# Performance work log

Measured on AMD Instinct MI355X. Metric: run time of the kernel, lower is better.

Reference implementation:

```python
import jax, jax.numpy as jnp
import numpy as np

INPUT_DIM = 10              # number of binary covariates in x
N = 2_000_000               # batch size
C = 2 ** (INPUT_DIM + 1)    # 2048 (t, x) combinations, one Linear(1,1) each


def setup_inputs() -> dict:
    key = jax.random.key(0)
    kx, kt, ky, kw, kb = jax.random.split(key, 5)
    x = jax.random.randint(kx, (N, INPUT_DIM), 0, 2).astype(jnp.float32)  # binary covariates
    t = jax.random.randint(kt, (N, 1), 0, 2).astype(jnp.float32)          # binary treatment
    y = jax.random.normal(ky, (N, 1), dtype=jnp.float32)                  # outcome
    # Per-combination Linear(1,1): weight w[i] and bias b[i] for q_z_dummies[i]
    w = jax.random.normal(kw, (C,), dtype=jnp.float32) * 0.5
    b = jax.random.normal(kb, (C,), dtype=jnp.float32) * 0.5
    return {"x": x, "t": t, "y": y, "w": w, "b": b}


def reference(x, t, y, w, b):
    # The torch loop sums (w_i*y + b_i) * [exact match of (t, x) with combination i].
    # Exactly one combination matches per row, so this equals a gather at the
    # combination index. itertools.product([0,1], repeat=d+1) orders bits
    # (t, x_0, ..., x_{d-1}) with the FIRST bit most significant.
    powers = (2 ** jnp.arange(INPUT_DIM - 1, -1, -1)).astype(x.dtype)      # [d]
    idx = (t[:, 0] * (2 ** INPUT_DIM) + x @ powers).astype(jnp.int32)      # [N]
    z_logits = y * w[idx][:, None] + b[idx][:, None]                       # [N, 1]
    # Original returns (z_mu=0, z_var=0, z_logits) in binary mode; z_logits is
    # the only tensor output.
    return z_logits
```

## Files before the change

kernel.cpp:

```cpp
#include <hip/hip_runtime.h>
#include <hip/hip_bf16.h>


#define D          10
#define C_TAB      2048
#define TILE_ROWS  128
#define BLOCKS     1024
#define WPB        4

__device__ __forceinline__ void async_load16(const void* g, void* l) {
    __builtin_amdgcn_global_load_lds(
        (const __attribute__((address_space(1))) void*)g,
        (__attribute__((address_space(3))) void*)l, 16, 0, 0);
}

__device__ __forceinline__ int make_idx(const float* row, float tt) {
    const float2* p = (const float2*)row;
    float2 a0 = p[0], a1 = p[1], a2 = p[2], a3 = p[3], a4 = p[4];
    float v = a0.x;
    v = fmaf(v, 2.f, a0.y);
    v = fmaf(v, 2.f, a1.x);
    v = fmaf(v, 2.f, a1.y);
    v = fmaf(v, 2.f, a2.x);
    v = fmaf(v, 2.f, a2.y);
    v = fmaf(v, 2.f, a3.x);
    v = fmaf(v, 2.f, a3.y);
    v = fmaf(v, 2.f, a4.x);
    v = fmaf(v, 2.f, a4.y);
    v = fmaf(tt, 1024.f, v);
    return (int)v;
}

__global__ __launch_bounds__(256, 4) void enc_kernel(
    const float* __restrict__ x,
    const float* __restrict__ t,
    const float* __restrict__ y,
    const float* __restrict__ w,
    const float* __restrict__ b,
    float* __restrict__ out,
    int nTiles, int nTotalWaves)
{
    __shared__ float lw[C_TAB];
    __shared__ float lb[C_TAB];
    __shared__ float xs[WPB][TILE_ROWS * D];

    const int tid = threadIdx.x;

    {
        const float4* w4 = (const float4*)w;
        const float4* b4 = (const float4*)b;
        float4* lw4 = (float4*)lw;
        float4* lb4 = (float4*)lb;
        lw4[tid]       = w4[tid];
        lw4[tid + 256] = w4[tid + 256];
        lb4[tid]       = b4[tid];
        lb4[tid + 256] = b4[tid + 256];
    }
    __syncthreads();

    const int wave = tid >> 6;
    const int lane = tid & 63;
    float* xw = xs[wave];

    for (int tile = blockIdx.x * WPB + wave; tile < nTiles; tile += nTotalWaves) {
        const char* gbase = (const char*)x + (size_t)tile * (TILE_ROWS * D * 4);
        #pragma unroll
        for (int k = 0; k < 5; ++k) {
            async_load16(gbase + k * 1024 + lane * 16, (char*)xw + k * 1024);
        }

        const int r0 = tile * TILE_ROWS + lane;
        const int r1 = r0 + 64;
        float t0 = t[r0], t1 = t[r1];
        float y0 = y[r0], y1 = y[r1];

        __builtin_amdgcn_s_waitcnt(0);
        __asm__ volatile("" ::: "memory");

        const int i0 = make_idx(&xw[lane * D], t0);
        const int i1 = make_idx(&xw[(lane + 64) * D], t1);

        out[r0] = fmaf(y0, lw[i0], lb[i0]);
        out[r1] = fmaf(y1, lw[i1], lb[i1]);
    }
}

__global__ __launch_bounds__(256) void enc_tail(
    const float* __restrict__ x, const float* __restrict__ t,
    const float* __restrict__ y, const float* __restrict__ w,
    const float* __restrict__ b, float* __restrict__ out,
    int start, int n)
{
    int i = start + blockIdx.x * blockDim.x + threadIdx.x;
    if (i >= n) return;
    const float* r = x + (size_t)i * D;
    float v = r[0];
    #pragma unroll
    for (int j = 1; j < D; ++j) v = fmaf(v, 2.f, r[j]);
    int idx = (int)fmaf(t[i], 1024.f, v);
    out[i] = fmaf(y[i], w[idx], b[idx]);
}

extern "C" void kernel_launch(void* const* d_in, const int* in_sizes, int n_in,
                              void* d_out, int out_size, void* d_ws, size_t ws_size,
                              hipStream_t stream) {
    const float* x = (const float*)d_in[0];
    const float* t = (const float*)d_in[1];
    const float* y = (const float*)d_in[2];
    const float* w = (const float*)d_in[3];
    const float* b = (const float*)d_in[4];
    float* out = (float*)d_out;

    const int n = out_size;
    const int nTiles = n / TILE_ROWS;
    const int rem = n - nTiles * TILE_ROWS;

    enc_kernel<<<BLOCKS, 256, 0, stream>>>(x, t, y, w, b, out,
                                           nTiles, BLOCKS * WPB);
    if (rem > 0) {
        enc_tail<<<(rem + 255) / 256, 256, 0, stream>>>(
            x, t, y, w, b, out, nTiles * TILE_ROWS, n);
    }
}
```

Before: 134.9 us.

## Double-buffer x tile DMA loads and interleave w/b into float2 table

Each wave now prefetches the next tile of x into a second LDS buffer, along with its t and y values, while it computes the current tile. It waits on a partial vmcnt so that only the current tile's loads must finish. The weight and bias tables are interleaved into one float2 LDS array, so each lookup is a single LDS read instead of two. The cost is doubled per-wave LDS use and more live registers, and the launch bounds hint drops from 4 to 2. The partial-wait count also relies on a fixed number of outstanding memory operations per iteration.

```diff
diff --git a/kernel.cpp b/kernel.cpp
--- a/kernel.cpp
+++ b/kernel.cpp
@@ -2,13 +2,16 @@
 #include <hip/hip_bf16.h>
 
 
-#define D          10
-#define C_TAB      2048
-#define TILE_ROWS  128
-#define BLOCKS     1024
-#define WPB        4
+#define D        10
+#define TILE     128
+#define WPB      4
+#define BLOCKS   1024
+#define NTHREADS 256
 
-__device__ __forceinline__ void async_load16(const void* g, void* l) {
+#define WAITCNT_VM9 0x0F79
+#define WAITCNT_VM0 0x0F70
+
+__device__ __forceinline__ void dma16(const void* g, void* l) {
     __builtin_amdgcn_global_load_lds(
         (const __attribute__((address_space(1))) void*)g,
         (__attribute__((address_space(3))) void*)l, 16, 0, 0);
@@ -31,57 +34,85 @@
     return (int)v;
 }
 
-__global__ __launch_bounds__(256, 4) void enc_kernel(
+__global__ __launch_bounds__(NTHREADS, 2) void enc_kernel(
     const float* __restrict__ x,
     const float* __restrict__ t,
     const float* __restrict__ y,
     const float* __restrict__ w,
     const float* __restrict__ b,
     float* __restrict__ out,
-    int nTiles, int nTotalWaves)
+    int nTiles, int stride)
 {
-    __shared__ float lw[C_TAB];
-    __shared__ float lb[C_TAB];
-    __shared__ float xs[WPB][TILE_ROWS * D];
+    __shared__ float2 lwb[2048];
+    __shared__ float xs[WPB][2][TILE * D];
 
     const int tid = threadIdx.x;
 
     {
         const float4* w4 = (const float4*)w;
         const float4* b4 = (const float4*)b;
-        float4* lw4 = (float4*)lw;
-        float4* lb4 = (float4*)lb;
-        lw4[tid]       = w4[tid];
-        lw4[tid + 256] = w4[tid + 256];
-        lb4[tid]       = b4[tid];
-        lb4[tid + 256] = b4[tid + 256];
+        #pragma unroll
+        for (int k = 0; k < 2; ++k) {
+            float4 fw = w4[tid * 2 + k];
+            float4 fb = b4[tid * 2 + k];
+            int base = (tid * 2 + k) * 4;
+            lwb[base + 0] = make_float2(fw.x, fb.x);
+            lwb[base + 1] = make_float2(fw.y, fb.y);
+            lwb[base + 2] = make_float2(fw.z, fb.z);
+            lwb[base + 3] = make_float2(fw.w, fb.w);
+        }
     }
     __syncthreads();
 
     const int wave = tid >> 6;
     const int lane = tid & 63;
-    float* xw = xs[wave];
+    float* bufs[2] = { xs[wave][0], xs[wave][1] };
 
-    for (int tile = blockIdx.x * WPB + wave; tile < nTiles; tile += nTotalWaves) {
-        const char* gbase = (const char*)x + (size_t)tile * (TILE_ROWS * D * 4);
+    int tile = blockIdx.x * WPB + wave;
+    if (tile >= nTiles) return;
+
+    {
+        const char* g = (const char*)x + (size_t)tile * (TILE * D * 4);
         #pragma unroll
-        for (int k = 0; k < 5; ++k) {
-            async_load16(gbase + k * 1024 + lane * 16, (char*)xw + k * 1024);
+        for (int k = 0; k < 5; ++k)
+            dma16(g + k * 1024 + lane * 16, (char*)bufs[0] + k * 1024);
+    }
+    int r0 = tile * TILE + lane;
+    float tc0 = t[r0], tc1 = t[r0 + 64];
+    float yc0 = y[r0], yc1 = y[r0 + 64];
+
+    int cb = 0;
+    while (tile < nTiles) {
+        const int next = tile + stride;
+        const bool hn = next < nTiles;
+        float tn0 = 0.f, tn1 = 0.f, yn0 = 0.f, yn1 = 0.f;
+        if (hn) {
+            const char* g = (const char*)x + (size_t)next * (TILE * D * 4);
+            #pragma unroll
+            for (int k = 0; k < 5; ++k)
+                dma16(g + k * 1024 + lane * 16, (char*)bufs[cb ^ 1] + k * 1024);
+            const int nr0 = next * TILE + lane;
+            tn0 = t[nr0]; tn1 = t[nr0 + 64];
+            yn0 = y[nr0]; yn1 = y[nr0 + 64];
         }
 
-        const int r0 = tile * TILE_ROWS + lane;
-        const int r1 = r0 + 64;
-        float t0 = t[r0], t1 = t[r1];
-        float y0 = y[r0], y1 = y[r1];
-
-        __builtin_amdgcn_s_waitcnt(0);
+        __asm__ volatile("" ::: "memory");
+        if (hn) __builtin_amdgcn_s_waitcnt(WAITCNT_VM9);
+        else    __builtin_amdgcn_s_waitcnt(WAITCNT_VM0);
         __asm__ volatile("" ::: "memory");
 
-        const int i0 = make_idx(&xw[lane * D], t0);
-        const int i1 = make_idx(&xw[(lane + 64) * D], t1);
+        const float* xw = bufs[cb];
+        const int i0 = make_idx(xw + lane * D, tc0);
+        const int i1 = make_idx(xw + (lane + 64) * D, tc1);
+        const float2 wb0 = lwb[i0];
+        const float2 wb1 = lwb[i1];
+        const int o0 = tile * TILE + lane;
+        out[o0]      = fmaf(yc0, wb0.x, wb0.y);
+        out[o0 + 64] = fmaf(yc1, wb1.x, wb1.y);
 
-        out[r0] = fmaf(y0, lw[i0], lb[i0]);
-        out[r1] = fmaf(y1, lw[i1], lb[i1]);
+        tile = next;
+        cb ^= 1;
+        tc0 = tn0; tc1 = tn1; yc0 = yn0; yc1 = yn1;
     }
 }
 
@@ -112,13 +143,13 @@
     float* out = (float*)d_out;
 
     const int n = out_size;
-    const int nTiles = n / TILE_ROWS;
-    const int rem = n - nTiles * TILE_ROWS;
+    const int nTiles = n / TILE;
+    const int rem = n - nTiles * TILE;
 
-    enc_kernel<<<BLOCKS, 256, 0, stream>>>(x, t, y, w, b, out,
-                                           nTiles, BLOCKS * WPB);
+    enc_kernel<<<BLOCKS, NTHREADS, 0, stream>>>(x, t, y, w, b, out,
+                                                nTiles, BLOCKS * WPB);
     if (rem > 0) {
         enc_tail<<<(rem + 255) / 256, 256, 0, stream>>>(
-            x, t, y, w, b, out, nTiles * TILE_ROWS, n);
+            x, t, y, w, b, out, nTiles * TILE, n);
     }
 }
```

Result: no change. 136.9 us (+1.5%).
